# Kernel tuning notes

Hardware: AMD Instinct MI355X
Metric: run time of the kernel (lower is better)

Reference implementation:

```python
import jax, jax.numpy as jnp
import numpy as np

B, SQ, SD, H = 64, 64, 512, 128


def setup_inputs() -> dict:
    key = jax.random.key(0)
    k1, k2, k3, k4, k5 = jax.random.split(key, 5)
    q = jax.random.normal(k1, (B, SQ, H), dtype=jnp.float32)
    d_pos = jax.random.normal(k2, (B, SD, H), dtype=jnp.float32)
    d_neg = jax.random.normal(k3, (B, SD, H), dtype=jnp.float32)
    mask_pos = jax.random.randint(k4, (B, SD), 0, 2, dtype=jnp.int32).at[:, 0].set(1)
    mask_neg = jax.random.randint(k5, (B, SD), 0, 2, dtype=jnp.int32).at[:, 0].set(1)
    return {"q": q, "d_pos": d_pos, "d_neg": d_neg,
            "mask_pos": mask_pos, "mask_neg": mask_neg}


def _colbert_maxsim(q, d, mask):
    # q: [a, s, h], d: [b, t, h], mask: [b, t] -> scores [a, b]
    simis = jnp.einsum('ash,bth->abst', q, d)            # [a, b, s, t]
    simis = jnp.where(mask[None, :, None, :] == 0, -jnp.inf, simis)
    return simis.max(axis=3).sum(axis=2)                 # max over t, sum over s


def reference(q, d_pos, d_neg, mask_pos, mask_neg):
    # Concatenate pos and in-batch-negative score blocks -> [B, 2B]
    distances = jnp.concatenate(
        [_colbert_maxsim(q, d_pos, mask_pos),
         _colbert_maxsim(q, d_neg, mask_neg)], axis=1)
    labels = jnp.arange(q.shape[0])
    logp = jax.nn.log_softmax(distances, axis=1)
    loss = -jnp.take_along_axis(logp, labels[:, None], axis=1).mean()
    return loss
```

## Files before the change

### kernel.cpp

```cpp
#include <hip/hip_runtime.h>
#include <hip/hip_bf16.h>
#include <math.h>
#include <stdint.h>

#define BB 64
#define SQN 64
#define SDN 512
#define HH 128

typedef __attribute__((ext_vector_type(8))) short bf16x8;
typedef __attribute__((ext_vector_type(16))) float f32x16;

__device__ __forceinline__ short f2bf(float f) {
  union { float f; unsigned u; } x; x.f = f;
  unsigned r = x.u + 0x7fffu + ((x.u >> 16) & 1u);
  return (short)(r >> 16);
}

__device__ __forceinline__ void gl_lds16(const short* g, short* l) {
  __builtin_amdgcn_global_load_lds(
      (const __attribute__((address_space(1))) unsigned int*)g,
      (__attribute__((address_space(3))) unsigned int*)l, 16, 0, 0);
}

__global__ __launch_bounds__(256)
void convert_all(const float* __restrict__ q, const float* __restrict__ dp,
                 const float* __restrict__ dn,
                 const int* __restrict__ mp, const int* __restrict__ mn,
                 short* __restrict__ oq, short* __restrict__ od,
                 int* __restrict__ nvalid, int* __restrict__ counter) {
  const int D_BLOCKS = (2 * BB * SDN) / 8;
  if (blockIdx.x < D_BLOCKS) {
    const int bs = blockIdx.x >> 6;
    const int j0 = (blockIdx.x & 63) * 8;
    const int side = bs >> 6, b = bs & 63;
    const int* mask = (side ? mn : mp) + b * SDN;

    __shared__ int s_perm[8];
    __shared__ int s_pad32;

    if (threadIdx.x < 64) {
      const int ln = threadIdx.x;
      int mreg[8];
      #pragma unroll
      for (int it = 0; it < 8; ++it) mreg[it] = mask[it * 64 + ln];
      int run = 0;
      #pragma unroll
      for (int it = 0; it < 8; ++it) {
        unsigned long long bal = __ballot(mreg[it] != 0);
        int pos = run + __popcll(bal & ((1ull << ln) - 1ull));
        if (mreg[it]) {
          unsigned rel = (unsigned)(pos - j0);
          if (rel < 8u) s_perm[rel] = it * 64 + ln;
        }
        run += (int)__popcll(bal);
      }
      if (ln < 8 && j0 + ln >= run) s_perm[ln] = -1;
      if (ln == 0) {
        s_pad32 = (run + 31) & ~31;
        if (j0 == 0) nvalid[bs] = run;
      }
    }
    __syncthreads();

    const int j = j0 + (threadIdx.x >> 5);
    if (j >= s_pad32) return;
    const int l32 = threadIdx.x & 31;
    const int src_t = s_perm[threadIdx.x >> 5];
    const float* srcmat = side ? dn : dp;
    float4 v = make_float4(0.f, 0.f, 0.f, 0.f);
    if (src_t >= 0)
      v = ((const float4*)(srcmat + ((size_t)b * SDN + src_t) * HH))[l32];
    short4 o; o.x = f2bf(v.x); o.y = f2bf(v.y); o.z = f2bf(v.z); o.w = f2bf(v.w);
    *(short4*)&od[((size_t)bs * SDN + j) * HH + l32 * 4] = o;
  } else {
    if (blockIdx.x == D_BLOCKS && threadIdx.x == 0) *counter = 0;
    int i = (blockIdx.x - D_BLOCKS) * 256 + threadIdx.x;
    float4 v = ((const float4*)q)[i];
    short4 o; o.x = f2bf(v.x); o.y = f2bf(v.y); o.z = f2bf(v.z); o.w = f2bf(v.w);
    *(short4*)&oq[i * 4] = o;
  }
}

__global__ __launch_bounds__(256, 2)
void maxsim_kernel(const short* __restrict__ qb,
                   const short* __restrict__ dc,
                   const int* __restrict__ nvalid,
                   float* __restrict__ scores,
                   int* __restrict__ counter,
                   float* __restrict__ out) {
  const int lid   = blockIdx.x + 32 * blockIdx.y;
  const int xcd   = lid & 7;
  const int slot  = lid >> 3;
  const int aslot = slot & 31;
  const int bs0   = (xcd + 8 * (slot >> 5)) * 4;

  __shared__ __align__(16) short d_lds[4][2][32 * 128];
  __shared__ float s_fin[4 * 2 * 2 * 32];
  __shared__ int s_ticket;
  __shared__ float part[16];

  const int tid = threadIdx.x;
  const int ln  = tid & 63;
  const int w   = tid >> 6;
  const int l31 = ln & 31;
  const int kh  = ln >> 5;

  int nvv[4], nch[4];
  #pragma unroll
  for (int i = 0; i < 4; ++i) {
    nvv[i] = nvalid[bs0 + i];
    nch[i] = (nvv[i] + 127) >> 7;
  }

  bf16x8 qf[2][2][8];
  #pragma unroll
  for (int qi = 0; qi < 2; ++qi) {
    #pragma unroll
    for (int half = 0; half < 2; ++half) {
      const short* qrow = qb + ((size_t)(aslot * 2 + qi) * SQN + half * 32 + l31) * HH + kh * 8;
      #pragma unroll
      for (int kc = 0; kc < 8; ++kc)
        qf[qi][half][kc] = *(const bf16x8*)(qrow + kc * 16);
    }
  }

  int src_off[8];
  {
    int r0 = ln >> 4, c0 = ln & 15;
    #pragma unroll
    for (int it = 0; it < 8; ++it) {
      int row_rel = it * 4 + r0;
      src_off[it] = row_rel * HH + (c0 ^ (row_rel & 15)) * 8;
    }
  }
  int rd_off[8];
  #pragma unroll
  for (int kc = 0; kc < 8; ++kc)
    rd_off[kc] = l31 * HH + (((kc * 2 + kh) ^ (l31 & 15)) * 8);

  float rmax[2][2] = {{0.f, 0.f}, {0.f, 0.f}};

  auto STAGE = [&](int pbi, int ptc, int rs) {
    const short* dsrc = dc + (((size_t)(bs0 + pbi) * SDN) + ptc * 128 + w * 32) * HH;
    short* slotp = &d_lds[w][rs][0];
    #pragma unroll
    for (int it = 0; it < 8; ++it)
      gl_lds16(dsrc + src_off[it], slotp + it * 512);
  };

  int pbi = 0, ptc = 0;
  STAGE(pbi, ptc, 0);
  if (++ptc == nch[pbi]) { ptc = 0; ++pbi; }

  int cbi = 0, ctc = 0, ring = 0;
  for (;;) {
    const bool hn = (pbi < 4);
    if (hn) {
      STAGE(pbi, ptc, ring ^ 1);
      if (++ptc == nch[pbi]) { ptc = 0; ++pbi; }
      asm volatile("s_waitcnt vmcnt(8)" ::: "memory");
    } else {
      asm volatile("s_waitcnt vmcnt(0)" ::: "memory");
    }

    const int rows = nvv[cbi] - (ctc << 7);
    if (w * 32 < rows) {
      const short* slotp = &d_lds[w][ring][0];
      bf16x8 dv[8];
      #pragma unroll
      for (int kc = 0; kc < 8; ++kc)
        dv[kc] = *(const bf16x8*)(slotp + rd_off[kc]);
      f32x16 a00 = {0,0,0,0,0,0,0,0,0,0,0,0,0,0,0,0};
      f32x16 a01 = {0,0,0,0,0,0,0,0,0,0,0,0,0,0,0,0};
      f32x16 a10 = {0,0,0,0,0,0,0,0,0,0,0,0,0,0,0,0};
      f32x16 a11 = {0,0,0,0,0,0,0,0,0,0,0,0,0,0,0,0};
      #pragma unroll
      for (int kc = 0; kc < 8; ++kc) {
        a00 = __builtin_amdgcn_mfma_f32_32x32x16_bf16(dv[kc], qf[0][0][kc], a00, 0, 0, 0);
        a01 = __builtin_amdgcn_mfma_f32_32x32x16_bf16(dv[kc], qf[0][1][kc], a01, 0, 0, 0);
        a10 = __builtin_amdgcn_mfma_f32_32x32x16_bf16(dv[kc], qf[1][0][kc], a10, 0, 0, 0);
        a11 = __builtin_amdgcn_mfma_f32_32x32x16_bf16(dv[kc], qf[1][1][kc], a11, 0, 0, 0);
      }
      float m00 = a00[0], m01 = a01[0], m10 = a10[0], m11 = a11[0];
      #pragma unroll
      for (int r = 1; r < 16; ++r) {
        m00 = fmaxf(m00, a00[r]);  m01 = fmaxf(m01, a01[r]);
        m10 = fmaxf(m10, a10[r]);  m11 = fmaxf(m11, a11[r]);
      }
      rmax[0][0] = fmaxf(rmax[0][0], m00);
      rmax[0][1] = fmaxf(rmax[0][1], m01);
      rmax[1][0] = fmaxf(rmax[1][0], m10);
      rmax[1][1] = fmaxf(rmax[1][1], m11);
    }

    const int obi = cbi;
    if (++ctc == nch[cbi]) {
      ctc = 0; ++cbi;
      float v[2][2];
      #pragma unroll
      for (int qi = 0; qi < 2; ++qi)
        #pragma unroll
        for (int half = 0; half < 2; ++half)
          v[qi][half] = fmaxf(rmax[qi][half], __shfl_xor(rmax[qi][half], 32));
      if (kh == 0) {
        #pragma unroll
        for (int qi = 0; qi < 2; ++qi)
          #pragma unroll
          for (int half = 0; half < 2; ++half)
            s_fin[((w * 2 + qi) * 2 + half) * 32 + l31] = v[qi][half];
      }
      asm volatile("s_waitcnt lgkmcnt(0)" ::: "memory");
      __builtin_amdgcn_s_barrier();
      if (w < 2) {
        float m0 = s_fin[((0 * 2 + w) * 2 + 0) * 32 + l31];
        float m1 = s_fin[((0 * 2 + w) * 2 + 1) * 32 + l31];
        #pragma unroll
        for (int ww = 1; ww < 4; ++ww) {
          m0 = fmaxf(m0, s_fin[((ww * 2 + w) * 2 + 0) * 32 + l31]);
          m1 = fmaxf(m1, s_fin[((ww * 2 + w) * 2 + 1) * 32 + l31]);
        }
        float s = m0 + m1;
        s += __shfl_xor(s, 1);  s += __shfl_xor(s, 2);  s += __shfl_xor(s, 4);
        s += __shfl_xor(s, 8);  s += __shfl_xor(s, 16);
        if (ln == 0)
          __hip_atomic_store(&scores[(size_t)(aslot * 2 + w) * (2 * BB) + bs0 + obi],
                             s, __ATOMIC_RELAXED, __HIP_MEMORY_SCOPE_AGENT);
      }
      __builtin_amdgcn_s_barrier();
      rmax[0][0] = 0.f; rmax[0][1] = 0.f; rmax[1][0] = 0.f; rmax[1][1] = 0.f;
    }

    if (cbi == 4) break;
    ring ^= 1;
  }

  asm volatile("s_waitcnt vmcnt(0)" ::: "memory");
  __syncthreads();
  if (tid == 0)
    s_ticket = __hip_atomic_fetch_add(counter, 1,
                                      __ATOMIC_RELAXED, __HIP_MEMORY_SCOPE_AGENT);
  __syncthreads();
  if (s_ticket != 1023) return;

  {
    #pragma unroll
    for (int q8 = 0; q8 < 4; ++q8) {
      int vp = w * 4 + q8;
      float acc = 0.f;
      #pragma unroll
      for (int i = 0; i < 4; ++i) {
        int r = vp * 4 + i;
        float v0 = __hip_atomic_load(&scores[r * 128 + ln],
                                     __ATOMIC_RELAXED, __HIP_MEMORY_SCOPE_AGENT);
        float v1 = __hip_atomic_load(&scores[r * 128 + 64 + ln],
                                     __ATOMIC_RELAXED, __HIP_MEMORY_SCOPE_AGENT);
        float mx = fmaxf(v0, v1);
        #pragma unroll
        for (int off = 32; off >= 1; off >>= 1) mx = fmaxf(mx, __shfl_xor(mx, off));
        float e = __expf(v0 - mx) + __expf(v1 - mx);
        #pragma unroll
        for (int off = 32; off >= 1; off >>= 1) e += __shfl_xor(e, off);
        float lse = mx + __logf(e);
        float diag = __shfl(v0, r);
        acc += lse - diag;
      }
      if (ln == 0) part[vp] = acc;
    }
  }
  __syncthreads();
  if (w == 0) {
    float v = (ln < 16) ? part[ln] : 0.f;
    #pragma unroll
    for (int off = 8; off >= 1; off >>= 1) v += __shfl_xor(v, off);
    if (ln == 0) out[0] = v * (1.0f / 64.0f);
  }
}

extern "C" void kernel_launch(void* const* d_in, const int* in_sizes, int n_in,
                              void* d_out, int out_size, void* d_ws, size_t ws_size,
                              hipStream_t stream) {
  const float* q        = (const float*)d_in[0];
  const float* d_pos    = (const float*)d_in[1];
  const float* d_neg    = (const float*)d_in[2];
  const int*   mask_pos = (const int*)d_in[3];
  const int*   mask_neg = (const int*)d_in[4];

  short* q_bf = (short*)d_ws;
  short* d_c  = q_bf + (size_t)BB * SQN * HH;
  int*   nvalid  = (int*)(d_c + (size_t)2 * BB * SDN * HH);
  float* scores  = (float*)(nvalid + 128);
  int*   counter = (int*)(scores + 64 * 128);

  const int D_BLOCKS = (2 * BB * SDN) / 8;
  const int Q_BLOCKS = (BB * SQN * HH / 4) / 256;
  convert_all<<<D_BLOCKS + Q_BLOCKS, 256, 0, stream>>>(
      q, d_pos, d_neg, mask_pos, mask_neg, q_bf, d_c, nvalid, counter);

  dim3 grid(32, 32);
  maxsim_kernel<<<grid, 256, 0, stream>>>(q_bf, d_c, nvalid, scores,
                                          counter, (float*)d_out);
}
```

Before: 141.5 us.

## Deepen LDS prefetch to two stages and batch score stores at kernel end

Prefetches two D chunks before the loop. Each iteration reads the current chunk into registers and then immediately reuses that LDS slot for the next prefetch, so two loads are always in flight. Per-block score stores now collect in shared memory and are written by one wave at the end, so the atomic global stores no longer sit inside the loop ahead of the barriers. Launch bounds switch to an explicit waves-per-EU attribute, and the tail issues dummy stages so the vmcnt(8) wait stays uniform, at the cost of some redundant loads.

After: 148.4 us. +4.8%, slower.

```diff
diff --git a/kernel.cpp b/kernel.cpp
--- a/kernel.cpp
+++ b/kernel.cpp
@@ -82,7 +82,8 @@
   }
 }
 
-__global__ __launch_bounds__(256, 2)
+__global__ __launch_bounds__(256)
+__attribute__((amdgpu_waves_per_eu(2, 2)))
 void maxsim_kernel(const short* __restrict__ qb,
                    const short* __restrict__ dc,
                    const int* __restrict__ nvalid,
@@ -97,6 +98,7 @@
 
   __shared__ __align__(16) short d_lds[4][2][32 * 128];
   __shared__ float s_fin[4 * 2 * 2 * 32];
+  __shared__ float s_out[8];
   __shared__ int s_ticket;
   __shared__ float part[16];
 
@@ -152,25 +154,32 @@
   int pbi = 0, ptc = 0;
   STAGE(pbi, ptc, 0);
   if (++ptc == nch[pbi]) { ptc = 0; ++pbi; }
+  STAGE(pbi, ptc, 1);
+  if (++ptc == nch[pbi]) { ptc = 0; ++pbi; }
 
   int cbi = 0, ctc = 0, ring = 0;
   for (;;) {
-    const bool hn = (pbi < 4);
-    if (hn) {
-      STAGE(pbi, ptc, ring ^ 1);
-      if (++ptc == nch[pbi]) { ptc = 0; ++pbi; }
-      asm volatile("s_waitcnt vmcnt(8)" ::: "memory");
-    } else {
-      asm volatile("s_waitcnt vmcnt(0)" ::: "memory");
-    }
+    asm volatile("s_waitcnt vmcnt(8)" ::: "memory");
 
     const int rows = nvv[cbi] - (ctc << 7);
-    if (w * 32 < rows) {
+    const bool act = (w * 32 < rows);
+    bf16x8 dv[8];
+    if (act) {
       const short* slotp = &d_lds[w][ring][0];
-      bf16x8 dv[8];
       #pragma unroll
       for (int kc = 0; kc < 8; ++kc)
         dv[kc] = *(const bf16x8*)(slotp + rd_off[kc]);
+    }
+    asm volatile("s_waitcnt lgkmcnt(0)" ::: "memory");
+
+    {
+      int qb2 = (pbi < 4) ? pbi : 0;
+      int qt2 = (pbi < 4) ? ptc : 0;
+      STAGE(qb2, qt2, ring);
+      if (pbi < 4) { if (++ptc == nch[pbi]) { ptc = 0; ++pbi; } }
+    }
+
+    if (act) {
       f32x16 a00 = {0,0,0,0,0,0,0,0,0,0,0,0,0,0,0,0};
       f32x16 a01 = {0,0,0,0,0,0,0,0,0,0,0,0,0,0,0,0};
       f32x16 a10 = {0,0,0,0,0,0,0,0,0,0,0,0,0,0,0,0};
@@ -223,10 +232,9 @@
         float s = m0 + m1;
         s += __shfl_xor(s, 1);  s += __shfl_xor(s, 2);  s += __shfl_xor(s, 4);
         s += __shfl_xor(s, 8);  s += __shfl_xor(s, 16);
-        if (ln == 0)
-          __hip_atomic_store(&scores[(size_t)(aslot * 2 + w) * (2 * BB) + bs0 + obi],
-                             s, __ATOMIC_RELAXED, __HIP_MEMORY_SCOPE_AGENT);
-      }
+        if (ln == 0) s_out[w * 4 + obi] = s;
+      }
+      asm volatile("s_waitcnt lgkmcnt(0)" ::: "memory");
       __builtin_amdgcn_s_barrier();
       rmax[0][0] = 0.f; rmax[0][1] = 0.f; rmax[1][0] = 0.f; rmax[1][1] = 0.f;
     }
@@ -235,8 +243,13 @@
     ring ^= 1;
   }
 
+  __syncthreads();
+  if (w == 0 && ln < 8) {
+    int qi = ln >> 2, bi = ln & 3;
+    __hip_atomic_store(&scores[(size_t)(aslot * 2 + qi) * (2 * BB) + bs0 + bi],
+                       s_out[ln], __ATOMIC_RELAXED, __HIP_MEMORY_SCOPE_AGENT);
+  }
   asm volatile("s_waitcnt vmcnt(0)" ::: "memory");
-  __syncthreads();
   if (tid == 0)
     s_ticket = __hip_atomic_fetch_add(counter, 1,
                                       __ATOMIC_RELAXED, __HIP_MEMORY_SCOPE_AGENT);
```
